# Kernel optimization log

Measured on AMD Instinct MI355X. Metric: run time of the kernel, lower is better.

The kernel has to match this reference:

```python
import jax, jax.numpy as jnp
import numpy as np

N_NODES = 50000
N_EDGES = 1600000
N_GRAPHS = 2048
DIM = 133
EPS = 1e-5


def gcn_conv(x, W, b, row, col, n_nodes):
    # PyG GCNConv: h = x @ W; add self-loops; sym-normalized scatter-add; + b
    h = x @ W  # [N, D]
    loops = jnp.arange(n_nodes, dtype=row.dtype)
    r = jnp.concatenate([row, loops])
    c = jnp.concatenate([col, loops])
    deg = jax.ops.segment_sum(jnp.ones_like(c, dtype=h.dtype), c, num_segments=n_nodes)
    dinv = jnp.where(deg > 0, jax.lax.rsqrt(deg), 0.0)
    norm = dinv[r] * dinv[c]  # [E+N]
    msg = h[r] * norm[:, None]  # gather + scale
    out = jax.ops.segment_sum(msg, c, num_segments=n_nodes)
    return out + b


def batchnorm_eval(x, gamma, beta, rm, rv):
    return (x - rm) * jax.lax.rsqrt(rv + EPS) * gamma + beta


def setup_inputs() -> dict:
    key = jax.random.key(0)
    ks = jax.random.split(key, 8)
    x = jax.random.normal(ks[0], (N_NODES, DIM), dtype=jnp.float32)
    edge_index = jax.random.randint(ks[1], (2, N_EDGES), 0, N_NODES, dtype=jnp.int64)
    batch = jnp.sort(jax.random.randint(ks[2], (N_NODES,), 0, N_GRAPHS, dtype=jnp.int64))
    s = 1.0 / np.sqrt(DIM)
    W1 = jax.random.uniform(ks[3], (DIM, DIM), jnp.float32, -s, s)
    W2 = jax.random.uniform(ks[4], (DIM, DIM), jnp.float32, -s, s)
    b1 = jnp.zeros((DIM,), jnp.float32)
    b2 = jnp.zeros((DIM,), jnp.float32)
    g1 = jnp.ones((DIM,), jnp.float32); beta1 = jnp.zeros((DIM,), jnp.float32)
    rm1 = jax.random.normal(ks[5], (DIM,), jnp.float32) * 0.1
    rv1 = jnp.ones((DIM,), jnp.float32)
    g2 = jnp.ones((DIM,), jnp.float32); beta2 = jnp.zeros((DIM,), jnp.float32)
    rm2 = jax.random.normal(ks[6], (DIM,), jnp.float32) * 0.1
    rv2 = jnp.ones((DIM,), jnp.float32)
    return {"x": x, "edge_index": edge_index, "batch": batch,
            "W1": W1, "b1": b1, "W2": W2, "b2": b2,
            "g1": g1, "beta1": beta1, "rm1": rm1, "rv1": rv1,
            "g2": g2, "beta2": beta2, "rm2": rm2, "rv2": rv2}


def reference(x, edge_index, batch, W1, b1, W2, b2,
              g1, beta1, rm1, rv1, g2, beta2, rm2, rv2):
    row, col = edge_index[0], edge_index[1]
    h = gcn_conv(x, W1, b1, row, col, N_NODES)
    h = jax.nn.relu(h)
    h = batchnorm_eval(h, g1, beta1, rm1, rv1)  # eval-mode BN; dropout is identity in eval
    h = gcn_conv(h, W2, b2, row, col, N_NODES)
    h = jax.nn.relu(h)
    h = batchnorm_eval(h, g2, beta2, rm2, rv2)
    # global mean pool per graph
    sums = jax.ops.segment_sum(h, batch, num_segments=N_GRAPHS)
    cnts = jax.ops.segment_sum(jnp.ones((N_NODES,), h.dtype), batch, num_segments=N_GRAPHS)
    return sums / jnp.maximum(cnts, 1.0)[:, None]
```

## Files before the change

kernel.cpp:

```cpp
#include <hip/hip_runtime.h>

#define N_NODES  50000
#define N_ROWS   50048
#define N_EDGES  1600000
#define N_GRAPHS 2048
#define DIM      133
#define HMSTR    128
#define HTSTR    8
#define YSTR     160
#define EPSV     1e-5f
#define NRANGE   16
#define RSPAN    3125
#define NSLICE   64
#define BUCKCAP  110000
#define EPB      1563
#define NPN      10

typedef __attribute__((ext_vector_type(8))) short bf16x8;
typedef __attribute__((ext_vector_type(4))) float f32x4;

__device__ __forceinline__ float blo(unsigned u) { return __uint_as_float(u << 16); }
__device__ __forceinline__ float bhi(unsigned u) { return __uint_as_float(u & 0xFFFF0000u); }
__device__ __forceinline__ unsigned short f2bf(float x) {
    unsigned v = __float_as_uint(x);
    return (unsigned short)((v + 0x7FFFu + ((v >> 16) & 1u)) >> 16);
}
__device__ __forceinline__ unsigned packbf(float a, float b) {
    return (unsigned)f2bf(a) | ((unsigned)f2bf(b) << 16);
}


__global__ __launch_bounds__(256) void k_part(const int* __restrict__ row,
                                              const int* __restrict__ col,
                                              int* __restrict__ bcnt,
                                              unsigned* __restrict__ buckets)
{
    __shared__ int cnt[NRANGE];
    __shared__ int cur[NRANGE];
    int e0 = blockIdx.x * EPB;
    if (threadIdx.x < NRANGE) cnt[threadIdx.x] = 0;
    __syncthreads();
    int e1 = min(e0 + EPB, N_EDGES);
    for (int e = e0 + threadIdx.x; e < e1; e += 256)
        atomicAdd(&cnt[col[e] / RSPAN], 1);
    __syncthreads();
    if (threadIdx.x < NRANGE)
        cur[threadIdx.x] = atomicAdd(&bcnt[threadIdx.x], cnt[threadIdx.x]);
    __syncthreads();
    for (int e = e0 + threadIdx.x; e < e1; e += 256) {
        int c = col[e];
        int r = c / RSPAN;
        int p = atomicAdd(&cur[r], 1);
        buckets[(size_t)r * BUCKCAP + p] =
            ((unsigned)row[e] << 12) | (unsigned)(c - r * RSPAN);
    }
}

__global__ __launch_bounds__(256) void k_count2(const unsigned* __restrict__ buckets,
                                                const int* __restrict__ bcnt,
                                                int* __restrict__ deg2)
{
    __shared__ int hist[RSPAN];
    int r = blockIdx.x & (NRANGE - 1);
    int s = blockIdx.x >> 4;
    int lo = r * RSPAN;
    for (int i = threadIdx.x; i < RSPAN; i += 256) hist[i] = 0;
    __syncthreads();
    int n = bcnt[r];
    int chunk = (n + NSLICE - 1) / NSLICE;
    int e0 = s * chunk, e1 = min(e0 + chunk, n);
    const unsigned* b = buckets + (size_t)r * BUCKCAP;
    for (int e = e0 + threadIdx.x; e < e1; e += 256)
        atomicAdd(&hist[b[e] & 0xFFFu], 1);
    __syncthreads();
    for (int i = threadIdx.x; i < RSPAN; i += 256)
        deg2[(size_t)s * N_NODES + lo + i] = hist[i];
}

__device__ __forceinline__ void w2bf_one(const float* __restrict__ W,
                                         unsigned short* __restrict__ Wbf, int idx)
{
    int j    = idx & 7;
    int lane = (idx >> 3) & 63;
    int kc   = (idx >> 9) % 5;
    int t    = idx / (8 * 64 * 5);
    int k = kc * 32 + (lane >> 4) * 8 + j;
    int n = t * 16 + (lane & 15);
    float v = (k < DIM && n < DIM) ? W[k * DIM + n] : 0.f;
    Wbf[idx] = f2bf(v);
}

#define X2BF_BLOCKS 15625

__global__ __launch_bounds__(256) void k_prep(const float* __restrict__ x,
                                              unsigned* __restrict__ Abf,
                                              const float* __restrict__ W1,
                                              const float* __restrict__ W2,
                                              unsigned short* __restrict__ Wbf1,
                                              unsigned short* __restrict__ Wbf2,
                                              const int* __restrict__ batch,
                                              float* __restrict__ inv_cnt)
{
    if (blockIdx.x < X2BF_BLOCKS) {
        int idx = blockIdx.x * 256 + threadIdx.x;
        if (idx >= N_NODES * 80) return;
        int r  = idx / 80;
        int c2 = (idx - r * 80) * 2;
        float a = (c2     < DIM) ? x[(size_t)r * DIM + c2]     : 0.f;
        float b = (c2 + 1 < DIM) ? x[(size_t)r * DIM + c2 + 1] : 0.f;
        Abf[idx] = packbf(a, b);
        return;
    }
    int tid = (blockIdx.x - X2BF_BLOCKS) * 256 + threadIdx.x;
    if (tid < 23040) {
        w2bf_one(W1, Wbf1, tid);
    } else if (tid < 46080) {
        w2bf_one(W2, Wbf2, tid - 23040);
    } else if (tid < 46080 + N_GRAPHS) {
        int g = tid - 46080;
        int a0 = 0, b0 = N_NODES;
        while (a0 < b0) { int m = (a0 + b0) >> 1; if (batch[m] < g) a0 = m + 1; else b0 = m; }
        int a1 = a0, b1 = N_NODES;
        while (a1 < b1) { int m = (a1 + b1) >> 1; if (batch[m] < g + 1) a1 = m + 1; else b1 = m; }
        inv_cnt[g] = 1.0f / (float)max(a1 - a0, 1);
    }
}

__global__ __launch_bounds__(256) void k_scan1(const int* __restrict__ deg2,
                                               float* __restrict__ dinv,
                                               int* __restrict__ offs,
                                               int* __restrict__ bsum)
{
    __shared__ int sd[256];
    int t = threadIdx.x;
    int idx = blockIdx.x * 256 + t;
    int v = 0;
    if (idx < N_NODES) {
        for (int s = 0; s < NSLICE; s++) v += deg2[(size_t)s * N_NODES + idx];
        dinv[idx] = rsqrtf((float)v + 1.0f);
    }
    sd[t] = v; __syncthreads();
    for (int o = 1; o < 256; o <<= 1) {
        int add = (t >= o) ? sd[t - o] : 0;
        __syncthreads();
        sd[t] += add;
        __syncthreads();
    }
    if (idx < N_NODES) offs[idx] = sd[t] - v;
    if (t == 255) bsum[blockIdx.x] = sd[255];
}

__global__ __launch_bounds__(256) void k_scan2(const int* __restrict__ bsum,
                                               int* __restrict__ boff, int nb)
{
    __shared__ int sd[256];
    int t = threadIdx.x;
    int v = (t < nb) ? bsum[t] : 0;
    sd[t] = v; __syncthreads();
    for (int o = 1; o < 256; o <<= 1) {
        int add = (t >= o) ? sd[t - o] : 0;
        __syncthreads();
        sd[t] += add;
        __syncthreads();
    }
    boff[t] = sd[t] - v;
}

__global__ __launch_bounds__(256) void k_scan3C(int* __restrict__ offs,
                                                const int* __restrict__ boff,
                                                int* __restrict__ deg2)
{
    int idx = blockIdx.x * 256 + threadIdx.x;
    if (idx < N_NODES) {
        int off = offs[idx] + boff[blockIdx.x];
        offs[idx] = off;
        int run = off;
        for (int s = 0; s < NSLICE; s++) {
            int d = deg2[(size_t)s * N_NODES + idx];
            deg2[(size_t)s * N_NODES + idx] = run;
            run += d;
        }
    } else if (idx == N_NODES) {
        offs[N_NODES] = N_EDGES;
    }
}

__global__ __launch_bounds__(256) void k_fill2(const unsigned* __restrict__ buckets,
                                               const int* __restrict__ bcnt,
                                               const int* __restrict__ offs2,
                                               const float* __restrict__ dinv,
                                               unsigned* __restrict__ csr)
{
    __shared__ int cur[RSPAN];
    int r = blockIdx.x & (NRANGE - 1);
    int s = blockIdx.x >> 4;
    int lo = r * RSPAN;
    for (int i = threadIdx.x; i < RSPAN; i += 256)
        cur[i] = offs2[(size_t)s * N_NODES + lo + i];
    __syncthreads();
    int n = bcnt[r];
    int chunk = (n + NSLICE - 1) / NSLICE;
    int e0 = s * chunk, e1 = min(e0 + chunk, n);
    const unsigned* b = buckets + (size_t)r * BUCKCAP;
    for (int e = e0 + threadIdx.x; e < e1; e += 256) {
        unsigned v = b[e];
        int src = (int)(v >> 12);
        int p = atomicAdd(&cur[v & 0xFFFu], 1);
        csr[p] = ((unsigned)src << 16) | (unsigned)f2bf(dinv[src]);
    }
}

__global__ __launch_bounds__(256) void k_gemm_mfma(const unsigned short* __restrict__ A,
                                                   const unsigned short* __restrict__ Wbf,
                                                   unsigned short* __restrict__ Hmain,
                                                   unsigned short* __restrict__ Htail, int M)
{
    int wave = threadIdx.x >> 6, lane = threadIdx.x & 63;
    int quad = lane >> 4, l16 = lane & 15;
    int m = blockIdx.x * 64 + wave * 16 + l16;

    const bf16x8* Arow = (const bf16x8*)(A + (size_t)m * YSTR);
    const bf16x8* Bq   = (const bf16x8*)Wbf;

    f32x4 acc[9] = {};
#pragma unroll
    for (int kc = 0; kc < 5; kc++) {
        bf16x8 af = Arow[kc * 4 + quad];
#pragma unroll
        for (int t = 0; t < 9; t++) {
            bf16x8 bfr = Bq[(t * 5 + kc) * 64 + lane];
            acc[t] = __builtin_amdgcn_mfma_f32_16x16x32_bf16(af, bfr, acc[t], 0, 0, 0);
        }
    }

    int gr0 = blockIdx.x * 64 + wave * 16 + quad * 4;
#pragma unroll
    for (int t = 0; t < 9; t++) {
        int c = t * 16 + l16;
#pragma unroll
        for (int reg = 0; reg < 4; reg++) {
            int gr = gr0 + reg;
            if (gr < M) {
                if (c < HMSTR) {
                    Hmain[(size_t)gr * HMSTR + c] = f2bf(acc[t][reg]);
                } else if (c < HMSTR + HTSTR) {
                    float v = (c < DIM) ? acc[t][reg] : 0.f;
                    Htail[(size_t)gr * HTSTR + (c - HMSTR)] = f2bf(v);
                }
            }
        }
    }
}


__device__ __forceinline__ void agg_row(const unsigned short* __restrict__ hmain,
                                        const unsigned short* __restrict__ htail,
                                        const int* __restrict__ offs,
                                        const unsigned* __restrict__ csr,
                                        const float* __restrict__ dinv,
                                        const float* __restrict__ bias,
                                        const float* __restrict__ gam,
                                        const float* __restrict__ bet,
                                        const float* __restrict__ rmean,
                                        const float* __restrict__ rvar,
                                        int node, int lane, int l2,
                                        float& va, float& vb, float& ta, float& tb)
{
    const unsigned* hm = (const unsigned*)hmain;
    const unsigned* ht = (const unsigned*)htail;

    float di = dinv[node];
    unsigned pw0 = hm[((size_t)node << 6) + lane];
    unsigned pw1 = ht[((unsigned)node << 2) + l2];
    float2 a0; a0.x = di * blo(pw0); a0.y = di * bhi(pw0);
    float2 a1; a1.x = di * blo(pw1); a1.y = di * bhi(pw1);

    int s0 = offs[node], s1 = offs[node + 1];
    int e = s0;
    for (; e + 8 <= s1; e += 8) {
        unsigned rec[8];
#pragma unroll
        for (int u = 0; u < 8; u++) rec[u] = csr[e + u];
        unsigned q0[8], q1[8];
#pragma unroll
        for (int u = 0; u < 8; u++) {
            unsigned src = rec[u] >> 16;
            q0[u] = hm[((size_t)src << 6) + lane];
            q1[u] = ht[(src << 2) + l2];
        }
#pragma unroll
        for (int u = 0; u < 8; u++) {
            float w = __uint_as_float(rec[u] << 16);
            a0.x += w * blo(q0[u]); a0.y += w * bhi(q0[u]);
            a1.x += w * blo(q1[u]); a1.y += w * bhi(q1[u]);
        }
    }
    for (; e < s1; e++) {
        unsigned rec = csr[e];
        unsigned src = rec >> 16;
        float w = __uint_as_float(rec << 16);
        unsigned q0 = hm[((size_t)src << 6) + lane];
        unsigned q1 = ht[(src << 2) + l2];
        a0.x += w * blo(q0); a0.y += w * bhi(q0);
        a1.x += w * blo(q1); a1.y += w * bhi(q1);
    }

    {
        int c = 2 * lane;
        float v = di * a0.x + bias[c];
        v = fmaxf(v, 0.f);
        va = (v - rmean[c]) * (gam[c] * rsqrtf(rvar[c] + EPSV)) + bet[c];
        int c1 = c + 1;
        v = di * a0.y + bias[c1];
        v = fmaxf(v, 0.f);
        vb = (v - rmean[c1]) * (gam[c1] * rsqrtf(rvar[c1] + EPSV)) + bet[c1];
    }
    ta = 0.f; tb = 0.f;
    if (lane < 4) {
        int c = 128 + 2 * l2;
        if (c < DIM) {
            float v = di * a1.x + bias[c];
            v = fmaxf(v, 0.f);
            ta = (v - rmean[c]) * (gam[c] * rsqrtf(rvar[c] + EPSV)) + bet[c];
        }
        int c1 = c + 1;
        if (c1 < DIM) {
            float v = di * a1.y + bias[c1];
            v = fmaxf(v, 0.f);
            tb = (v - rmean[c1]) * (gam[c1] * rsqrtf(rvar[c1] + EPSV)) + bet[c1];
        }
    }
}

template <bool FINAL>
__global__ __launch_bounds__(256) void k_agg(const unsigned short* __restrict__ hmain,
                                             const unsigned short* __restrict__ htail,
                                             const int* __restrict__ offs,
                                             const unsigned* __restrict__ csr,
                                             const float* __restrict__ dinv,
                                             const float* __restrict__ bias,
                                             const float* __restrict__ gam,
                                             const float* __restrict__ bet,
                                             const float* __restrict__ rmean,
                                             const float* __restrict__ rvar,
                                             unsigned short* __restrict__ y,
                                             const int* __restrict__ batch,
                                             const float* __restrict__ inv_cnt,
                                             float* __restrict__ outp)
{
    int lane = threadIdx.x & 63;
    int l2 = lane & 3;

    if (!FINAL) {
        int node = __builtin_amdgcn_readfirstlane(blockIdx.x * 4 + (threadIdx.x >> 6));
        if (node >= N_NODES) return;
        float va, vb, ta, tb;
        agg_row(hmain, htail, offs, csr, dinv, bias, gam, bet, rmean, rvar,
                node, lane, l2, va, vb, ta, tb);
        ((unsigned*)(y + (size_t)node * YSTR))[lane] = packbf(va, vb);
        if (lane < 16)
            ((unsigned*)(y + (size_t)node * YSTR))[64 + lane] =
                (lane < 4) ? packbf(ta, tb) : 0u;
        return;
    }

    int node0 = __builtin_amdgcn_readfirstlane((blockIdx.x * 4 + (threadIdx.x >> 6)) * NPN);
    if (node0 >= N_NODES) return;
    int nend = min(node0 + NPN, N_NODES);

    float p0x = 0.f, p0y = 0.f, p1x = 0.f, p1y = 0.f;
    int curg = batch[node0];

    for (int node = node0; node < nend; node++) {
        int bg = batch[node];
        if (bg != curg) {
            float ic = inv_cnt[curg];
            int c = 2 * lane;
            atomicAdd(&outp[(size_t)curg * DIM + c],     p0x * ic);
            atomicAdd(&outp[(size_t)curg * DIM + c + 1], p0y * ic);
            if (lane < 4) {
                int ct = 128 + 2 * l2;
                if (ct     < DIM) atomicAdd(&outp[(size_t)curg * DIM + ct],     p1x * ic);
                if (ct + 1 < DIM) atomicAdd(&outp[(size_t)curg * DIM + ct + 1], p1y * ic);
            }
            p0x = p0y = p1x = p1y = 0.f;
            curg = bg;
        }
        float va, vb, ta, tb;
        agg_row(hmain, htail, offs, csr, dinv, bias, gam, bet, rmean, rvar,
                node, lane, l2, va, vb, ta, tb);
        p0x += va; p0y += vb; p1x += ta; p1y += tb;
    }
    {
        float ic = inv_cnt[curg];
        int c = 2 * lane;
        atomicAdd(&outp[(size_t)curg * DIM + c],     p0x * ic);
        atomicAdd(&outp[(size_t)curg * DIM + c + 1], p0y * ic);
        if (lane < 4) {
            int ct = 128 + 2 * l2;
            if (ct     < DIM) atomicAdd(&outp[(size_t)curg * DIM + ct],     p1x * ic);
            if (ct + 1 < DIM) atomicAdd(&outp[(size_t)curg * DIM + ct + 1], p1y * ic);
        }
    }
}


extern "C" void kernel_launch(void* const* d_in, const int* in_sizes, int n_in,
                              void* d_out, int out_size, void* d_ws, size_t ws_size,
                              hipStream_t stream)
{
    const float* x   = (const float*)d_in[0];
    const int*   ei  = (const int*)d_in[1];
    const int*   bat = (const int*)d_in[2];
    const float* W1  = (const float*)d_in[3];
    const float* b1  = (const float*)d_in[4];
    const float* W2  = (const float*)d_in[5];
    const float* b2  = (const float*)d_in[6];
    const float* g1  = (const float*)d_in[7];
    const float* be1 = (const float*)d_in[8];
    const float* rm1 = (const float*)d_in[9];
    const float* rv1 = (const float*)d_in[10];
    const float* g2  = (const float*)d_in[11];
    const float* be2 = (const float*)d_in[12];
    const float* rm2 = (const float*)d_in[13];
    const float* rv2 = (const float*)d_in[14];
    float* outp = (float*)d_out;
    char* ws = (char*)d_ws;

    int*   bcnt    = (int*)  (ws + 0);
    int*   offs    = (int*)  (ws + 200000);
    float* dinv    = (float*)(ws + 400016);
    float* inv_cnt = (float*)(ws + 600016);
    int*   bsum    = (int*)  (ws + 608208);
    int*   boff    = (int*)  (ws + 609232);
    unsigned* csr  = (unsigned*)(ws + 610256);
    unsigned short* Wbf1 = (unsigned short*)(ws + 7010256);
    unsigned short* Wbf2 = (unsigned short*)(ws + 7056336);
    unsigned short* Abf  = (unsigned short*)(ws + 7102416);
    unsigned short* Y1   = Abf;
    unsigned short* Hm   = (unsigned short*)(ws + 23118080);
    unsigned short* Ht   = (unsigned short*)(ws + 35930368);
    unsigned* buckets = (unsigned*)(ws + 23118080);
    int*      deg2    = (int*)    (ws + 30158080);

    hipMemsetAsync(bcnt, 0, 64, stream);
    hipMemsetAsync(d_out, 0, (size_t)out_size * 4, stream);

    const int* row = ei;
    const int* col = ei + N_EDGES;

    int nbl = (N_NODES + 255) / 256;

    k_part  <<<dim3(1024), dim3(256), 0, stream>>>(row, col, bcnt, buckets);
    k_prep  <<<dim3(X2BF_BLOCKS + 189), dim3(256), 0, stream>>>(x, (unsigned*)Abf,
                                                                W1, W2, Wbf1, Wbf2,
                                                                bat, inv_cnt);
    k_count2<<<dim3(NSLICE * NRANGE), dim3(256), 0, stream>>>(buckets, bcnt, deg2);
    k_scan1 <<<dim3(nbl), dim3(256), 0, stream>>>(deg2, dinv, offs, bsum);
    k_scan2 <<<dim3(1),   dim3(256), 0, stream>>>(bsum, boff, nbl);
    k_scan3C<<<dim3(nbl), dim3(256), 0, stream>>>(offs, boff, deg2);
    k_fill2 <<<dim3(NSLICE * NRANGE), dim3(256), 0, stream>>>(buckets, bcnt, deg2, dinv, csr);

    int gbl = N_ROWS / 64;
    k_gemm_mfma<<<dim3(gbl), dim3(256), 0, stream>>>(Abf, Wbf1, Hm, Ht, N_NODES);
    k_agg<false><<<dim3(N_NODES / 4), dim3(256), 0, stream>>>(Hm, Ht, offs, csr, dinv,
                                                              b1, g1, be1, rm1, rv1,
                                                              Y1, nullptr, nullptr, nullptr);
    k_gemm_mfma<<<dim3(gbl), dim3(256), 0, stream>>>(Y1, Wbf2, Hm, Ht, N_NODES);
    int fbl = (N_NODES + 4 * NPN - 1) / (4 * NPN);
    k_agg<true><<<dim3(fbl), dim3(256), 0, stream>>>(Hm, Ht, offs, csr, dinv,
                                                     b2, g2, be2, rm2, rv2,
                                                     nullptr, bat, inv_cnt, outp);
}
```

Baseline: 326.0 us.

## Split aggregation into column-half and tail blocks with deeper gather unrolling

The aggregation kernels now give each wave one 64-column half of a node's feature row, or the 5-column tail, in separate block ranges. Before, one wave handled all 133 columns together. The main-half gathers are unrolled by 16 with a 4-wide remainder loop, BN parameters are hoisted out of the per-node loop, and the final pooling kernel works on 4 nodes per wave instead of 10. This is meant to raise memory-level parallelism and occupancy for the irregular gathers. The cost is that CSR indices and dinv are read three times, half the lanes sit idle during half-row work, and the pooling stage issues more atomics.

```diff
diff --git a/kernel.cpp b/kernel.cpp
--- a/kernel.cpp
+++ b/kernel.cpp
@@ -14,7 +14,12 @@
 #define NSLICE   64
 #define BUCKCAP  110000
 #define EPB      1563
-#define NPN      10
+#define NPN      4
+
+#define NBH  12500
+#define NBT  12500
+#define NBF  3125
+#define NBFT 3125
 
 typedef __attribute__((ext_vector_type(8))) short bf16x8;
 typedef __attribute__((ext_vector_type(4))) float f32x4;
@@ -253,27 +258,64 @@
 }
 
 
-__device__ __forceinline__ void agg_row(const unsigned short* __restrict__ hmain,
-                                        const unsigned short* __restrict__ htail,
-                                        const int* __restrict__ offs,
-                                        const unsigned* __restrict__ csr,
-                                        const float* __restrict__ dinv,
-                                        const float* __restrict__ bias,
-                                        const float* __restrict__ gam,
-                                        const float* __restrict__ bet,
-                                        const float* __restrict__ rmean,
-                                        const float* __restrict__ rvar,
-                                        int node, int lane, int l2,
-                                        float& va, float& vb, float& ta, float& tb)
-{
-    const unsigned* hm = (const unsigned*)hmain;
-    const unsigned* ht = (const unsigned*)htail;
-
+__device__ __forceinline__ float2 agg_half(const unsigned* __restrict__ hmw,
+                                           const int* __restrict__ offs,
+                                           const unsigned* __restrict__ csr,
+                                           const float* __restrict__ dinv,
+                                           int node, int woff)
+{
     float di = dinv[node];
-    unsigned pw0 = hm[((size_t)node << 6) + lane];
-    unsigned pw1 = ht[((unsigned)node << 2) + l2];
-    float2 a0; a0.x = di * blo(pw0); a0.y = di * bhi(pw0);
-    float2 a1; a1.x = di * blo(pw1); a1.y = di * bhi(pw1);
+    unsigned qs = hmw[((size_t)node << 6) + woff];
+    float2 a; a.x = di * blo(qs); a.y = di * bhi(qs);
+
+    int s0 = offs[node], s1 = offs[node + 1];
+    int e = s0;
+    for (; e + 16 <= s1; e += 16) {
+        unsigned rec[16];
+#pragma unroll
+        for (int u = 0; u < 16; u++) rec[u] = csr[e + u];
+        unsigned q[16];
+#pragma unroll
+        for (int u = 0; u < 16; u++)
+            q[u] = hmw[((size_t)(rec[u] >> 16) << 6) + woff];
+#pragma unroll
+        for (int u = 0; u < 16; u++) {
+            float w = __uint_as_float(rec[u] << 16);
+            a.x += w * blo(q[u]); a.y += w * bhi(q[u]);
+        }
+    }
+    for (; e + 4 <= s1; e += 4) {
+        unsigned rec[4];
+#pragma unroll
+        for (int u = 0; u < 4; u++) rec[u] = csr[e + u];
+        unsigned q[4];
+#pragma unroll
+        for (int u = 0; u < 4; u++)
+            q[u] = hmw[((size_t)(rec[u] >> 16) << 6) + woff];
+#pragma unroll
+        for (int u = 0; u < 4; u++) {
+            float w = __uint_as_float(rec[u] << 16);
+            a.x += w * blo(q[u]); a.y += w * bhi(q[u]);
+        }
+    }
+    for (; e < s1; e++) {
+        unsigned rec = csr[e];
+        float w = __uint_as_float(rec << 16);
+        unsigned q = hmw[((size_t)(rec >> 16) << 6) + woff];
+        a.x += w * blo(q); a.y += w * bhi(q);
+    }
+    return a;
+}
+
+__device__ __forceinline__ float2 agg_tail(const unsigned* __restrict__ htw,
+                                           const int* __restrict__ offs,
+                                           const unsigned* __restrict__ csr,
+                                           const float* __restrict__ dinv,
+                                           int node, int l2)
+{
+    float di = dinv[node];
+    unsigned qs = htw[((unsigned)node << 2) + l2];
+    float2 a; a.x = di * blo(qs); a.y = di * bhi(qs);
 
     int s0 = offs[node], s1 = offs[node + 1];
     int e = s0;
@@ -281,55 +323,39 @@
         unsigned rec[8];
 #pragma unroll
         for (int u = 0; u < 8; u++) rec[u] = csr[e + u];
-        unsigned q0[8], q1[8];
-#pragma unroll
-        for (int u = 0; u < 8; u++) {
-            unsigned src = rec[u] >> 16;
-            q0[u] = hm[((size_t)src << 6) + lane];
-            q1[u] = ht[(src << 2) + l2];
-        }
+        unsigned q[8];
+#pragma unroll
+        for (int u = 0; u < 8; u++)
+            q[u] = htw[((rec[u] >> 16) << 2) + l2];
 #pragma unroll
         for (int u = 0; u < 8; u++) {
             float w = __uint_as_float(rec[u] << 16);
-            a0.x += w * blo(q0[u]); a0.y += w * bhi(q0[u]);
-            a1.x += w * blo(q1[u]); a1.y += w * bhi(q1[u]);
+            a.x += w * blo(q[u]); a.y += w * bhi(q[u]);
         }
     }
     for (; e < s1; e++) {
         unsigned rec = csr[e];
-        unsigned src = rec >> 16;
         float w = __uint_as_float(rec << 16);
-        unsigned q0 = hm[((size_t)src << 6) + lane];
-        unsigned q1 = ht[(src << 2) + l2];
-        a0.x += w * blo(q0); a0.y += w * bhi(q0);
-        a1.x += w * blo(q1); a1.y += w * bhi(q1);
-    }
-
-    {
-        int c = 2 * lane;
-        float v = di * a0.x + bias[c];
-        v = fmaxf(v, 0.f);
-        va = (v - rmean[c]) * (gam[c] * rsqrtf(rvar[c] + EPSV)) + bet[c];
-        int c1 = c + 1;
-        v = di * a0.y + bias[c1];
-        v = fmaxf(v, 0.f);
-        vb = (v - rmean[c1]) * (gam[c1] * rsqrtf(rvar[c1] + EPSV)) + bet[c1];
-    }
-    ta = 0.f; tb = 0.f;
-    if (lane < 4) {
-        int c = 128 + 2 * l2;
-        if (c < DIM) {
-            float v = di * a1.x + bias[c];
-            v = fmaxf(v, 0.f);
-            ta = (v - rmean[c]) * (gam[c] * rsqrtf(rvar[c] + EPSV)) + bet[c];
-        }
-        int c1 = c + 1;
-        if (c1 < DIM) {
-            float v = di * a1.y + bias[c1];
-            v = fmaxf(v, 0.f);
-            tb = (v - rmean[c1]) * (gam[c1] * rsqrtf(rvar[c1] + EPSV)) + bet[c1];
-        }
-    }
+        unsigned q = htw[((rec >> 16) << 2) + l2];
+        a.x += w * blo(q); a.y += w * bhi(q);
+    }
+    return a;
+}
+
+__device__ __forceinline__ void bnp(int c, const float* __restrict__ bias,
+                                    const float* __restrict__ gam,
+                                    const float* __restrict__ bet,
+                                    const float* __restrict__ rmean,
+                                    const float* __restrict__ rvar,
+                                    float& bb, float& rm, float& sc, float& bt)
+{
+    bb = bias[c]; rm = rmean[c]; sc = gam[c] * rsqrtf(rvar[c] + EPSV); bt = bet[c];
+}
+__device__ __forceinline__ float bnap(float acc, float di, float bb, float rm,
+                                      float sc, float bt)
+{
+    float v = fmaxf(di * acc + bb, 0.f);
+    return (v - rm) * sc + bt;
 }
 
 template <bool FINAL>
@@ -349,58 +375,117 @@
                                              float* __restrict__ outp)
 {
     int lane = threadIdx.x & 63;
-    int l2 = lane & 3;
+    int wv   = threadIdx.x >> 6;
+    int l5   = lane & 31;
+    int l2   = lane & 3;
+    const unsigned* hmw = (const unsigned*)hmain;
+    const unsigned* htw = (const unsigned*)htail;
+    int b = blockIdx.x;
 
     if (!FINAL) {
-        int node = __builtin_amdgcn_readfirstlane(blockIdx.x * 4 + (threadIdx.x >> 6));
-        if (node >= N_NODES) return;
-        float va, vb, ta, tb;
-        agg_row(hmain, htail, offs, csr, dinv, bias, gam, bet, rmean, rvar,
-                node, lane, l2, va, vb, ta, tb);
-        ((unsigned*)(y + (size_t)node * YSTR))[lane] = packbf(va, vb);
-        if (lane < 16)
-            ((unsigned*)(y + (size_t)node * YSTR))[64 + lane] =
-                (lane < 4) ? packbf(ta, tb) : 0u;
+        if (b < 2 * NBH) {
+            int h = (b >= NBH) ? 1 : 0;
+            int node = __builtin_amdgcn_readfirstlane((h ? b - NBH : b) * 4 + wv);
+            int woff = h * 32 + l5;
+            int c = h * 64 + 2 * l5;
+            float bb0, rm0, sc0, bt0, bb1, rm1, sc1, bt1;
+            bnp(c,     bias, gam, bet, rmean, rvar, bb0, rm0, sc0, bt0);
+            bnp(c + 1, bias, gam, bet, rmean, rvar, bb1, rm1, sc1, bt1);
+            float2 a = agg_half(hmw, offs, csr, dinv, node, woff);
+            float di = dinv[node];
+            float va = bnap(a.x, di, bb0, rm0, sc0, bt0);
+            float vb = bnap(a.y, di, bb1, rm1, sc1, bt1);
+            if (lane < 32)
+                ((unsigned*)(y + (size_t)node * YSTR))[woff] = packbf(va, vb);
+        } else {
+            int node = __builtin_amdgcn_readfirstlane((b - 2 * NBH) * 4 + wv);
+            float2 a = agg_tail(htw, offs, csr, dinv, node, l2);
+            float di = dinv[node];
+            float ta = 0.f, tb = 0.f;
+            if (lane < 4) {
+                int c = 128 + 2 * l2;
+                if (c < DIM) {
+                    float bb, rm, sc, bt;
+                    bnp(c, bias, gam, bet, rmean, rvar, bb, rm, sc, bt);
+                    ta = bnap(a.x, di, bb, rm, sc, bt);
+                }
+                if (c + 1 < DIM) {
+                    float bb, rm, sc, bt;
+                    bnp(c + 1, bias, gam, bet, rmean, rvar, bb, rm, sc, bt);
+                    tb = bnap(a.y, di, bb, rm, sc, bt);
+                }
+            }
+            if (lane < 16)
+                ((unsigned*)(y + (size_t)node * YSTR))[64 + lane] =
+                    (lane < 4) ? packbf(ta, tb) : 0u;
+        }
         return;
     }
 
-    int node0 = __builtin_amdgcn_readfirstlane((blockIdx.x * 4 + (threadIdx.x >> 6)) * NPN);
-    if (node0 >= N_NODES) return;
-    int nend = min(node0 + NPN, N_NODES);
-
-    float p0x = 0.f, p0y = 0.f, p1x = 0.f, p1y = 0.f;
-    int curg = batch[node0];
-
-    for (int node = node0; node < nend; node++) {
-        int bg = batch[node];
-        if (bg != curg) {
-            float ic = inv_cnt[curg];
-            int c = 2 * lane;
-            atomicAdd(&outp[(size_t)curg * DIM + c],     p0x * ic);
-            atomicAdd(&outp[(size_t)curg * DIM + c + 1], p0y * ic);
-            if (lane < 4) {
-                int ct = 128 + 2 * l2;
-                if (ct     < DIM) atomicAdd(&outp[(size_t)curg * DIM + ct],     p1x * ic);
-                if (ct + 1 < DIM) atomicAdd(&outp[(size_t)curg * DIM + ct + 1], p1y * ic);
+    if (b < 2 * NBF) {
+        int h = (b >= NBF) ? 1 : 0;
+        int node0 = __builtin_amdgcn_readfirstlane(((h ? b - NBF : b) * 4 + wv) * NPN);
+        int woff = h * 32 + l5;
+        int c = h * 64 + 2 * l5;
+        float bb0, rm0, sc0, bt0, bb1, rm1, sc1, bt1;
+        bnp(c,     bias, gam, bet, rmean, rvar, bb0, rm0, sc0, bt0);
+        bnp(c + 1, bias, gam, bet, rmean, rvar, bb1, rm1, sc1, bt1);
+
+        float px = 0.f, py = 0.f;
+        int curg = batch[node0];
+#pragma unroll
+        for (int k = 0; k < NPN; k++) {
+            int node = node0 + k;
+            int bg = batch[node];
+            if (bg != curg) {
+                float ic = inv_cnt[curg];
+                if (lane < 32) {
+                    atomicAdd(&outp[(size_t)curg * DIM + c],     px * ic);
+                    atomicAdd(&outp[(size_t)curg * DIM + c + 1], py * ic);
+                }
+                px = py = 0.f;
+                curg = bg;
             }
-            p0x = p0y = p1x = p1y = 0.f;
-            curg = bg;
-        }
-        float va, vb, ta, tb;
-        agg_row(hmain, htail, offs, csr, dinv, bias, gam, bet, rmean, rvar,
-                node, lane, l2, va, vb, ta, tb);
-        p0x += va; p0y += vb; p1x += ta; p1y += tb;
-    }
-    {
+            float2 a = agg_half(hmw, offs, csr, dinv, node, woff);
+            float di = dinv[node];
+            px += bnap(a.x, di, bb0, rm0, sc0, bt0);
+            py += bnap(a.y, di, bb1, rm1, sc1, bt1);
+        }
         float ic = inv_cnt[curg];
-        int c = 2 * lane;
-        atomicAdd(&outp[(size_t)curg * DIM + c],     p0x * ic);
-        atomicAdd(&outp[(size_t)curg * DIM + c + 1], p0y * ic);
-        if (lane < 4) {
-            int ct = 128 + 2 * l2;
-            if (ct     < DIM) atomicAdd(&outp[(size_t)curg * DIM + ct],     p1x * ic);
-            if (ct + 1 < DIM) atomicAdd(&outp[(size_t)curg * DIM + ct + 1], p1y * ic);
-        }
+        if (lane < 32) {
+            atomicAdd(&outp[(size_t)curg * DIM + c],     px * ic);
+            atomicAdd(&outp[(size_t)curg * DIM + c + 1], py * ic);
+        }
+    } else {
+        int node0 = __builtin_amdgcn_readfirstlane(((b - 2 * NBF) * 4 + wv) * NPN);
+        int c = 128 + 2 * l2;
+        bool v0 = (lane < 4) && (c < DIM);
+        bool v1 = (lane < 4) && (c + 1 < DIM);
+        float bb0 = 0, rm0 = 0, sc0 = 0, bt0 = 0, bb1 = 0, rm1 = 0, sc1 = 0, bt1 = 0;
+        if (v0) bnp(c,     bias, gam, bet, rmean, rvar, bb0, rm0, sc0, bt0);
+        if (v1) bnp(c + 1, bias, gam, bet, rmean, rvar, bb1, rm1, sc1, bt1);
+
+        float px = 0.f, py = 0.f;
+        int curg = batch[node0];
+#pragma unroll
+        for (int k = 0; k < NPN; k++) {
+            int node = node0 + k;
+            int bg = batch[node];
+            if (bg != curg) {
+                float ic = inv_cnt[curg];
+                if (v0) atomicAdd(&outp[(size_t)curg * DIM + c],     px * ic);
+                if (v1) atomicAdd(&outp[(size_t)curg * DIM + c + 1], py * ic);
+                px = py = 0.f;
+                curg = bg;
+            }
+            float2 a = agg_tail(htw, offs, csr, dinv, node, l2);
+            float di = dinv[node];
+            if (v0) px += bnap(a.x, di, bb0, rm0, sc0, bt0);
+            if (v1) py += bnap(a.y, di, bb1, rm1, sc1, bt1);
+        }
+        float ic = inv_cnt[curg];
+        if (v0) atomicAdd(&outp[(size_t)curg * DIM + c],     px * ic);
+        if (v1) atomicAdd(&outp[(size_t)curg * DIM + c + 1], py * ic);
     }
 }
 
@@ -463,12 +548,11 @@
 
     int gbl = N_ROWS / 64;
     k_gemm_mfma<<<dim3(gbl), dim3(256), 0, stream>>>(Abf, Wbf1, Hm, Ht, N_NODES);
-    k_agg<false><<<dim3(N_NODES / 4), dim3(256), 0, stream>>>(Hm, Ht, offs, csr, dinv,
-                                                              b1, g1, be1, rm1, rv1,
-                                                              Y1, nullptr, nullptr, nullptr);
+    k_agg<false><<<dim3(2 * NBH + NBT), dim3(256), 0, stream>>>(Hm, Ht, offs, csr, dinv,
+                                                                b1, g1, be1, rm1, rv1,
+                                                                Y1, nullptr, nullptr, nullptr);
     k_gemm_mfma<<<dim3(gbl), dim3(256), 0, stream>>>(Y1, Wbf2, Hm, Ht, N_NODES);
-    int fbl = (N_NODES + 4 * NPN - 1) / (4 * NPN);
-    k_agg<true><<<dim3(fbl), dim3(256), 0, stream>>>(Hm, Ht, offs, csr, dinv,
-                                                     b2, g2, be2, rm2, rv2,
-                                                     nullptr, bat, inv_cnt, outp);
-}
+    k_agg<true><<<dim3(2 * NBF + NBFT), dim3(256), 0, stream>>>(Hm, Ht, offs, csr, dinv,
+                                                                b2, g2, be2, rm2, rv2,
+                                                                nullptr, bat, inv_cnt, outp);
+}
```

Result: slower. 357.2 us (+9.6%).
